# Kernel tuning notes

Measured on AMD Instinct MI355X. Metric: run time of the kernel, lower is better.

The kernel has to match this reference:

```python
import jax, jax.numpy as jnp
import numpy as np

B, S, D_IN, D_OUT = 4, 4096, 1024, 1024

def setup_inputs() -> dict:
    key = jax.random.key(0)
    kx, kq, kk, kv = jax.random.split(key, 4)
    # torch Linear weights are [out, in]; init scale ~ U(-1/sqrt(in), 1/sqrt(in))
    lim = 1.0 / np.sqrt(D_IN)
    x = jax.random.normal(kx, (B, S, D_IN), dtype=jnp.float32)
    W_query = jax.random.uniform(kq, (D_OUT, D_IN), dtype=jnp.float32, minval=-lim, maxval=lim)
    W_key = jax.random.uniform(kk, (D_OUT, D_IN), dtype=jnp.float32, minval=-lim, maxval=lim)
    W_value = jax.random.uniform(kv, (D_OUT, D_IN), dtype=jnp.float32, minval=-lim, maxval=lim)
    return {"x": x, "W_query": W_query, "W_key": W_key, "W_value": W_value}

def reference(x, W_query, W_key, W_value):
    # Linear: x @ W.T  (torch convention, weight shape [out, in])
    q = jnp.einsum('bsd,od->bso', x, W_query)
    k = jnp.einsum('bsd,od->bso', x, W_key)
    v = jnp.einsum('bsd,od->bso', x, W_value)
    scale = 1.0 / jnp.sqrt(jnp.asarray(k.shape[-1], dtype=x.dtype))
    scores = jnp.einsum('bqo,bko->bqk', q, k) * scale  # [B,S,S]
    weights = jax.nn.softmax(scores, axis=-1)
    return jnp.einsum('bqk,bko->bqo', weights, v)  # [B,S,D_OUT]
```

## Files before the change

### kernel.cpp

```cpp
#include <hip/hip_runtime.h>
#include <cstdint>
#include <cstddef>

typedef __attribute__((ext_vector_type(8))) short short8;
typedef __attribute__((ext_vector_type(4))) float f32x4;

__device__ __forceinline__ unsigned short f2bf(float x) {
  union { float f; unsigned u; } v; v.f = x;
  unsigned r = (v.u + 0x7FFFu + ((v.u >> 16) & 1u)) >> 16;
  return (unsigned short)r;
}

#define GLOAD16(g, l)                                                    \
  __builtin_amdgcn_global_load_lds(                                      \
      (const __attribute__((address_space(1))) unsigned int*)(g),        \
      (__attribute__((address_space(3))) unsigned int*)(l), 16, 0, 0)

#define DSR(dst, addrv, imm)                                             \
  asm volatile("ds_read_b128 %0, %1 offset:%c2"                          \
               : "=&v"(dst) : "v"(addrv), "i"(imm))

__global__ __launch_bounds__(256) void cvt_all(
    const float* __restrict__ x, unsigned short* __restrict__ xb,
    const float* __restrict__ wq, const float* __restrict__ wk,
    unsigned short* __restrict__ wqT, unsigned short* __restrict__ wkT,
    const float* __restrict__ wv, unsigned short* __restrict__ wvb) {
  __shared__ float tile[64][65];
  int b = blockIdx.x;
  int t = threadIdx.x;
  if (b < 8192) {
    long i = ((long)b * 256 + t) * 8;
    const float4* p = (const float4*)(x + i);
    float4 a = p[0], c = p[1];
    short8 r;
    r[0] = (short)f2bf(a.x); r[1] = (short)f2bf(a.y);
    r[2] = (short)f2bf(a.z); r[3] = (short)f2bf(a.w);
    r[4] = (short)f2bf(c.x); r[5] = (short)f2bf(c.y);
    r[6] = (short)f2bf(c.z); r[7] = (short)f2bf(c.w);
    *(short8*)(xb + i) = r;
  } else if (b < 8704) {
    int tb = b - 8192;
    const float* in = (tb & 256) ? wk : wq;
    unsigned short* out = (tb & 256) ? wkT : wqT;
    int tb2 = tb & 255;
    int O0 = (tb2 >> 4) * 64;
    int I0 = (tb2 & 15) * 64;
    int r0 = t >> 6, c = t & 63;
#pragma unroll
    for (int r = 0; r < 16; r++) {
      int row = r * 4 + r0;
      tile[row][c] = in[(size_t)(O0 + row) * 1024 + I0 + c];
    }
    __syncthreads();
#pragma unroll
    for (int r = 0; r < 16; r++) {
      int irow = r * 4 + r0;
      out[(size_t)(I0 + irow) * 1024 + O0 + c] = f2bf(tile[c][irow]);
    }
  } else {
    long i = ((long)(b - 8704) * 256 + t) * 8;
    const float4* p = (const float4*)(wv + i);
    float4 a = p[0], c = p[1];
    short8 r;
    r[0] = (short)f2bf(a.x); r[1] = (short)f2bf(a.y);
    r[2] = (short)f2bf(a.z); r[3] = (short)f2bf(a.w);
    r[4] = (short)f2bf(c.x); r[5] = (short)f2bf(c.y);
    r[6] = (short)f2bf(c.z); r[7] = (short)f2bf(c.w);
    *(short8*)(wvb + i) = r;
  }
}

__global__ __launch_bounds__(256) void reduce_rsum(
    const float* __restrict__ part, float* __restrict__ outr,
    size_t stride, int n) {
  int i = blockIdx.x * 256 + threadIdx.x;
  if (i >= n) return;
  float s = 0.f;
#pragma unroll
  for (int p = 0; p < 64; p++) s += part[(size_t)p * stride + i];
  outr[i] = 1.0f / s;
}

__global__ __launch_bounds__(256) void gemm128(
    const unsigned short* __restrict__ A, int lda,
    const unsigned short* __restrict__ B, int ldb,
    unsigned short* __restrict__ C, int ldc,
    int nbn, int K, float scale) {
  __shared__ unsigned short As[128 * 64];
  __shared__ unsigned short Bs[128 * 64];

  unsigned bid = blockIdx.x;
  unsigned cpx = gridDim.x >> 3;
  unsigned swz = (bid & 7u) * cpx + (bid >> 3);
  int bm = (int)(swz / (unsigned)nbn);
  int bn = (int)(swz % (unsigned)nbn);
  int m0 = bm * 128, n0 = bn * 128;

  int t = threadIdx.x;
  int lane = t & 63, wid = t >> 6;
  int wm = wid >> 1, wn = wid & 1;
  int l15 = lane & 15, l4 = lane >> 4;

  int srow = t >> 3;
  int g = (t & 7) ^ ((t >> 3) & 7);
  const unsigned short* pa = A + (size_t)(m0 + srow) * lda + g * 8;
  const unsigned short* pb = B + (size_t)(n0 + srow) * ldb + g * 8;

  f32x4 acc[4][4] = {};

  for (int k0 = 0; k0 < K; k0 += 64) {
    __syncthreads();
#pragma unroll
    for (int i = 0; i < 4; i++) {
      GLOAD16(pa + (size_t)(32 * i) * lda + k0,
              (char*)As + (size_t)(i * 256 + wid * 64) * 16);
      GLOAD16(pb + (size_t)(32 * i) * ldb + k0,
              (char*)Bs + (size_t)(i * 256 + wid * 64) * 16);
    }
    __syncthreads();
#pragma unroll
    for (int ks = 0; ks < 2; ks++) {
      short8 af[4], bfr[4];
#pragma unroll
      for (int mi = 0; mi < 4; mi++) {
        int r = wm * 64 + mi * 16 + l15;
        int c = ((ks << 2) | l4) ^ (r & 7);
        af[mi] = *(const short8*)((const char*)As + r * 128 + c * 16);
      }
#pragma unroll
      for (int ni = 0; ni < 4; ni++) {
        int r = wn * 64 + ni * 16 + l15;
        int c = ((ks << 2) | l4) ^ (r & 7);
        bfr[ni] = *(const short8*)((const char*)Bs + r * 128 + c * 16);
      }
#pragma unroll
      for (int mi = 0; mi < 4; mi++)
#pragma unroll
        for (int ni = 0; ni < 4; ni++)
          acc[mi][ni] = __builtin_amdgcn_mfma_f32_16x16x32_bf16(
              af[mi], bfr[ni], acc[mi][ni], 0, 0, 0);
    }
  }

#pragma unroll
  for (int mi = 0; mi < 4; mi++)
#pragma unroll
    for (int ni = 0; ni < 4; ni++)
#pragma unroll
      for (int j = 0; j < 4; j++) {
        int row = m0 + wm * 64 + mi * 16 + l4 * 4 + j;
        int col = n0 + wn * 64 + ni * 16 + l15;
        C[(size_t)row * ldc + col] = f2bf(acc[mi][ni][j] * scale);
      }
}

template <int MODE>
__device__ __forceinline__ void gemm_body(
    unsigned short (*As)[256 * 64], unsigned short (*Bs)[256 * 64],
    const unsigned short* __restrict__ A, int lda,
    const unsigned short* __restrict__ B, int ldb,
    void* __restrict__ Cb, int ldc,
    float* __restrict__ rs, size_t rsp,
    int nbn, int K, float scale, int stile) {
  unsigned bid = blockIdx.x;
  int bm, bn;
  if (stile) {
    unsigned xcd = bid & 7u, idx = bid >> 3;
    bm = (int)((xcd >> 1) * 4 + (idx & 3));
    bn = (int)((xcd & 1) * 8 + (idx >> 2));
  } else {
    unsigned cpx = gridDim.x >> 3;
    unsigned swz = (bid & 7u) * cpx + (bid >> 3);
    bm = (int)(swz / (unsigned)nbn);
    bn = (int)(swz % (unsigned)nbn);
  }
  int m0 = bm * 256, n0 = bn * 256;

  int t512 = threadIdx.x;
  int lane = t512 & 63, wid = t512 >> 6;
  int wm = wid >> 2, wn = wid & 3;
  int l15 = lane & 15, l4 = lane >> 4;

  int srow = t512 >> 3;
  int g = (t512 & 7) ^ ((t512 >> 3) & 7);
  const unsigned short* pa = A + (size_t)(m0 + srow) * lda + g * 8;
  const unsigned short* pb = B + (size_t)(n0 + srow) * ldb + g * 8;

  f32x4 acc[8][4] = {};

  const int NT = K >> 6;

#define STAGE(jj, buf)                                                    \
  do {                                                                    \
    int _k0 = (jj) << 6;                                                  \
    _Pragma("unroll") for (int i = 0; i < 4; i++)                         \
        GLOAD16(pa + (size_t)(i * 64) * lda + _k0,                        \
                (char*)As[buf] + i * 8192 + t512 * 16);                   \
    _Pragma("unroll") for (int i = 0; i < 4; i++)                         \
        GLOAD16(pb + (size_t)(i * 64) * ldb + _k0,                        \
                (char*)Bs[buf] + i * 8192 + t512 * 16);                   \
  } while (0)

  unsigned c0 = ((unsigned)l4) ^ (unsigned)(l15 & 7);
  unsigned c1 = (4u | (unsigned)l4) ^ (unsigned)(l15 & 7);
  unsigned rowA = (unsigned)(wm * 128 + l15) * 128u;
  unsigned rowB = (unsigned)(wn * 64 + l15) * 128u;

  STAGE(0, 0);

  for (int j = 0; j < NT; ++j) {
    int cur = j & 1;
    __builtin_amdgcn_sched_barrier(0);
    __builtin_amdgcn_s_barrier();
    if (j + 1 < NT) {
      STAGE(j + 1, cur ^ 1);
      asm volatile("s_waitcnt vmcnt(8)" ::: "memory");
    } else {
      asm volatile("s_waitcnt vmcnt(0)" ::: "memory");
    }
    __builtin_amdgcn_s_barrier();

    unsigned baseA = (unsigned)(uintptr_t)(
        (__attribute__((address_space(3))) char*)(&As[cur][0]));
    unsigned baseB = (unsigned)(uintptr_t)(
        (__attribute__((address_space(3))) char*)(&Bs[cur][0]));
    unsigned aA0 = baseA + rowA + c0 * 16, aA1 = baseA + rowA + c1 * 16;
    unsigned aB0 = baseB + rowB + c0 * 16, aB1 = baseB + rowB + c1 * 16;

    short8 afq[2][2][2];
    short8 bfv[4][2];

    DSR(afq[0][0][0], aA0, 0);
    DSR(afq[0][0][1], aA1, 0);
    DSR(afq[0][1][0], aA0, 2048);
    DSR(afq[0][1][1], aA1, 2048);
#pragma unroll
    for (int ni = 0; ni < 4; ni++) {
      DSR(bfv[ni][0], aB0, ni * 2048);
      DSR(bfv[ni][1], aB1, ni * 2048);
    }

#pragma unroll
    for (int p = 0; p < 4; ++p) {
      if (p < 3) {
        const int mi0 = (p + 1) * 2;
        DSR(afq[(p + 1) & 1][0][0], aA0, mi0 * 2048);
        DSR(afq[(p + 1) & 1][0][1], aA1, mi0 * 2048);
        DSR(afq[(p + 1) & 1][1][0], aA0, (mi0 + 1) * 2048);
        DSR(afq[(p + 1) & 1][1][1], aA1, (mi0 + 1) * 2048);
        asm volatile("s_waitcnt lgkmcnt(4)" ::: "memory");
      } else {
        asm volatile("s_waitcnt lgkmcnt(0)" ::: "memory");
      }
      __builtin_amdgcn_sched_barrier(0);
      __builtin_amdgcn_s_setprio(1);
#pragma unroll
      for (int ks = 0; ks < 2; ks++)
#pragma unroll
        for (int m2 = 0; m2 < 2; m2++) {
          int mi = p * 2 + m2;
#pragma unroll
          for (int ni = 0; ni < 4; ni++)
            acc[mi][ni] = __builtin_amdgcn_mfma_f32_16x16x32_bf16(
                afq[p & 1][m2][ks], bfv[ni][ks], acc[mi][ni], 0, 0, 0);
        }
      __builtin_amdgcn_s_setprio(0);
      __builtin_amdgcn_sched_barrier(0);
    }
  }
#undef STAGE

  if constexpr (MODE == 2) {
    float sums[8][4];
#pragma unroll
    for (int mi = 0; mi < 8; mi++)
#pragma unroll
      for (int jj = 0; jj < 4; jj++) sums[mi][jj] = 0.f;
#pragma unroll
    for (int mi = 0; mi < 8; mi++)
#pragma unroll
      for (int ni = 0; ni < 4; ni++)
#pragma unroll
        for (int jj = 0; jj < 4; jj++) {
          int row = m0 + wm * 128 + mi * 16 + l4 * 4 + jj;
          int col = n0 + wn * 64 + ni * 16 + l15;
          float e = __expf(acc[mi][ni][jj] * scale);
          sums[mi][jj] += e;
          ((unsigned short*)Cb)[(size_t)row * ldc + col] = f2bf(e);
        }
    size_t pslot = (size_t)(bn * 4 + wn) * rsp;
#pragma unroll
    for (int mi = 0; mi < 8; mi++)
#pragma unroll
      for (int jj = 0; jj < 4; jj++) {
        float s = sums[mi][jj];
        s += __shfl_xor(s, 1);
        s += __shfl_xor(s, 2);
        s += __shfl_xor(s, 4);
        s += __shfl_xor(s, 8);
        if (l15 == 0) {
          int row = m0 + wm * 128 + mi * 16 + l4 * 4 + jj;
          rs[pslot + row] = s;
        }
      }
  } else {
#pragma unroll
    for (int mi = 0; mi < 8; mi++) {
      float inv[4];
      if constexpr (MODE == 3) {
#pragma unroll
        for (int jj = 0; jj < 4; jj++) {
          int row = m0 + wm * 128 + mi * 16 + l4 * 4 + jj;
          inv[jj] = rs[row];
        }
      }
#pragma unroll
      for (int ni = 0; ni < 4; ni++)
#pragma unroll
        for (int jj = 0; jj < 4; jj++) {
          int row = m0 + wm * 128 + mi * 16 + l4 * 4 + jj;
          int col = n0 + wn * 64 + ni * 16 + l15;
          float val = acc[mi][ni][jj];
          if constexpr (MODE == 1)
            ((unsigned short*)Cb)[(size_t)row * ldc + col] = f2bf(val * scale);
          else
            ((float*)Cb)[(size_t)row * ldc + col] = val * inv[jj];
        }
    }
  }
}

template <int MODE, int STILE>
__global__ __launch_bounds__(512, 2) void gemm_bt256(
    const unsigned short* __restrict__ A, int lda, size_t asb,
    const unsigned short* __restrict__ B, int ldb, size_t bsb,
    void* __restrict__ C, int ldc, size_t csb,
    float* __restrict__ rs, int rss, size_t rsp,
    int nbn, int K, float scale) {
  __shared__ unsigned short As[2][256 * 64];
  __shared__ unsigned short Bs[2][256 * 64];
  gemm_body<MODE>(As, Bs,
                  A + (size_t)blockIdx.y * asb, lda,
                  B + (size_t)blockIdx.y * bsb, ldb,
                  (char*)C + (size_t)blockIdx.y * csb * (MODE == 3 ? 4 : 2),
                  ldc, rs + (size_t)blockIdx.y * rss, rsp, nbn, K, scale,
                  STILE);
}

__global__ __launch_bounds__(512, 2) void gemm_dual(
    const unsigned short* __restrict__ A0, int lda0,
    const unsigned short* __restrict__ B0, int ldb0,
    void* __restrict__ C0, int ldc0, int nbn0,
    const unsigned short* __restrict__ A1, int lda1,
    const unsigned short* __restrict__ B1, int ldb1,
    void* __restrict__ C1, int ldc1, int nbn1, int K) {
  __shared__ unsigned short As[2][256 * 64];
  __shared__ unsigned short Bs[2][256 * 64];
  if (blockIdx.y == 0)
    gemm_body<1>(As, Bs, A0, lda0, B0, ldb0, C0, ldc0, nullptr, 0, nbn0, K,
                 1.0f, 0);
  else
    gemm_body<1>(As, Bs, A1, lda1, B1, ldb1, C1, ldc1, nullptr, 0, nbn1, K,
                 1.0f, 0);
}

extern "C" void kernel_launch(void* const* d_in, const int* in_sizes, int n_in,
                              void* d_out, int out_size, void* d_ws, size_t ws_size,
                              hipStream_t stream) {
  (void)in_sizes; (void)n_in; (void)out_size;
  const float* x  = (const float*)d_in[0];
  const float* Wq = (const float*)d_in[1];
  const float* Wk = (const float*)d_in[2];
  const float* Wv = (const float*)d_in[3];
  float* out = (float*)d_out;

  const int Bn = 4, S = 4096, D = 1024;
  const size_t MS = (size_t)Bn * S;
  const float scale = 0.03125f;

  char* ws = (char*)d_ws;
  unsigned short* xb  = (unsigned short*)ws; ws += MS * D * 2;
  unsigned short* xMb = (unsigned short*)ws; ws += MS * D * 2;
  unsigned short* VTb = (unsigned short*)ws; ws += MS * D * 2;
  unsigned short* Sreg = (unsigned short*)ws;
  const size_t s4_bytes = (size_t)Bn * S * S * 2;
  const size_t s1_bytes = (size_t)S * S * 2;
  size_t head = (size_t)(ws - (char*)d_ws);
  bool batched = ws_size >= head + s4_bytes + 16u * 1024 * 1024;
  ws += batched ? s4_bytes : s1_bytes;
  unsigned short* wqT = (unsigned short*)ws; ws += (size_t)D * D * 2;
  unsigned short* wkT = (unsigned short*)ws; ws += (size_t)D * D * 2;
  unsigned short* MTb = (unsigned short*)ws; ws += (size_t)D * D * 2;
  unsigned short* wvb = (unsigned short*)ws; ws += (size_t)D * D * 2;
  float* rpart = (float*)ws; ws += 64 * MS * sizeof(float);
  float* rinv  = (float*)ws;

  cvt_all<<<9216, 256, 0, stream>>>(x, xb, Wq, Wk, wqT, wkT, Wv, wvb);

  gemm128<<<64, 256, 0, stream>>>(wkT, D, wqT, D, MTb, D, 8, D, 1.0f);

  gemm_dual<<<dim3(256, 2), 512, 0, stream>>>(
      wvb, D, xb, D, VTb, (int)MS, 64,
      xb, D, MTb, D, xMb, D, 4, D);

  if (batched) {
    gemm_bt256<2, 1><<<dim3(256, Bn), 512, 0, stream>>>(
        xMb, D, (size_t)S * D,
        xb, D, (size_t)S * D,
        Sreg, S, (size_t)S * S, rpart, S, MS, 16, D, scale);
    reduce_rsum<<<(int)(MS / 256), 256, 0, stream>>>(rpart, rinv, MS, (int)MS);
    gemm_bt256<3, 0><<<dim3(64, Bn), 512, 0, stream>>>(
        Sreg, S, (size_t)S * S,
        VTb, (int)MS, (size_t)S,
        out, D, (size_t)S * D, rinv, S, 0, 4, S, 1.0f);
  } else {
    for (int b = 0; b < Bn; b++) {
      gemm_bt256<2, 1><<<dim3(256, 1), 512, 0, stream>>>(
          xMb + (size_t)b * S * D, D, 0,
          xb + (size_t)b * S * D, D, 0,
          Sreg, S, 0, rpart + (size_t)b * S, 0, MS, 16, D, scale);
      reduce_rsum<<<S / 256, 256, 0, stream>>>(
          rpart + (size_t)b * S, rinv + (size_t)b * S, MS, S);
      gemm_bt256<3, 0><<<dim3(64, 1), 512, 0, stream>>>(
          Sreg, S, 0, VTb + (size_t)b * S, (int)MS, 0,
          out + (size_t)b * S * D, D, 0, rinv + (size_t)b * S, 0, 0,
          4, S, 1.0f);
    }
  }
}
```

Baseline: 398.3 us.

## Split-K the weight-product GEMM into eight partial blocks plus reduction

The 1024x1024 Wk^T·Wq product previously ran as a single 64-block GEMM that underfilled the GPU. It now splits K into eight 128-wide chunks across a second grid dimension, writes fp32 partials into the score scratch region, and sums them in a separate reduction kernel that converts to bf16. This raises parallelism at the cost of an extra launch and 32 MB of partial-sum traffic. The result also moves from a single fp32 accumulation to an fp32 sum of partials.

```diff
diff --git a/kernel.cpp b/kernel.cpp
--- a/kernel.cpp
+++ b/kernel.cpp
@@ -3,6 +3,7 @@
 #include <cstddef>
 
 typedef __attribute__((ext_vector_type(8))) short short8;
+typedef __attribute__((ext_vector_type(4))) short short4v;
 typedef __attribute__((ext_vector_type(4))) float f32x4;
 
 __device__ __forceinline__ unsigned short f2bf(float x) {
@@ -81,20 +82,21 @@
   outr[i] = 1.0f / s;
 }
 
-__global__ __launch_bounds__(256) void gemm128(
-    const unsigned short* __restrict__ A, int lda,
-    const unsigned short* __restrict__ B, int ldb,
-    unsigned short* __restrict__ C, int ldc,
-    int nbn, int K, float scale) {
+__global__ __launch_bounds__(256) void mt_part(
+    const unsigned short* __restrict__ A,
+    const unsigned short* __restrict__ B,
+    float* __restrict__ P) {
   __shared__ unsigned short As[128 * 64];
   __shared__ unsigned short Bs[128 * 64];
+  const int lda = 1024, ldb = 1024;
 
   unsigned bid = blockIdx.x;
   unsigned cpx = gridDim.x >> 3;
   unsigned swz = (bid & 7u) * cpx + (bid >> 3);
-  int bm = (int)(swz / (unsigned)nbn);
-  int bn = (int)(swz % (unsigned)nbn);
+  int bm = (int)(swz >> 3);
+  int bn = (int)(swz & 7u);
   int m0 = bm * 128, n0 = bn * 128;
+  int kbase = (int)blockIdx.y << 7;
 
   int t = threadIdx.x;
   int lane = t & 63, wid = t >> 6;
@@ -103,12 +105,12 @@
 
   int srow = t >> 3;
   int g = (t & 7) ^ ((t >> 3) & 7);
-  const unsigned short* pa = A + (size_t)(m0 + srow) * lda + g * 8;
-  const unsigned short* pb = B + (size_t)(n0 + srow) * ldb + g * 8;
+  const unsigned short* pa = A + (size_t)(m0 + srow) * lda + g * 8 + kbase;
+  const unsigned short* pb = B + (size_t)(n0 + srow) * ldb + g * 8 + kbase;
 
   f32x4 acc[4][4] = {};
 
-  for (int k0 = 0; k0 < K; k0 += 64) {
+  for (int k0 = 0; k0 < 128; k0 += 64) {
     __syncthreads();
 #pragma unroll
     for (int i = 0; i < 4; i++) {
@@ -142,6 +144,7 @@
     }
   }
 
+  float* out = P + (size_t)blockIdx.y * 1048576;
 #pragma unroll
   for (int mi = 0; mi < 4; mi++)
 #pragma unroll
@@ -150,8 +153,23 @@
       for (int j = 0; j < 4; j++) {
         int row = m0 + wm * 64 + mi * 16 + l4 * 4 + j;
         int col = n0 + wn * 64 + ni * 16 + l15;
-        C[(size_t)row * ldc + col] = f2bf(acc[mi][ni][j] * scale);
-      }
+        out[(size_t)row * 1024 + col] = acc[mi][ni][j];
+      }
+}
+
+__global__ __launch_bounds__(256) void mt_reduce(
+    const float* __restrict__ P, unsigned short* __restrict__ M) {
+  size_t i = ((size_t)blockIdx.x * 256 + threadIdx.x) * 4;
+  float4 s = *(const float4*)(P + i);
+#pragma unroll
+  for (int c = 1; c < 8; c++) {
+    float4 v = *(const float4*)(P + (size_t)c * 1048576 + i);
+    s.x += v.x; s.y += v.y; s.z += v.z; s.w += v.w;
+  }
+  short4v r;
+  r[0] = (short)f2bf(s.x); r[1] = (short)f2bf(s.y);
+  r[2] = (short)f2bf(s.z); r[3] = (short)f2bf(s.w);
+  *(short4v*)(M + i) = r;
 }
 
 template <int MODE>
@@ -394,10 +412,12 @@
   unsigned short* wvb = (unsigned short*)ws; ws += (size_t)D * D * 2;
   float* rpart = (float*)ws; ws += 64 * MS * sizeof(float);
   float* rinv  = (float*)ws;
+  float* mtp = (float*)Sreg;
 
   cvt_all<<<9216, 256, 0, stream>>>(x, xb, Wq, Wk, wqT, wkT, Wv, wvb);
 
-  gemm128<<<64, 256, 0, stream>>>(wkT, D, wqT, D, MTb, D, 8, D, 1.0f);
+  mt_part<<<dim3(64, 8), 256, 0, stream>>>(wkT, wqT, mtp);
+  mt_reduce<<<1024, 256, 0, stream>>>(mtp, MTb);
 
   gemm_dual<<<dim3(256, 2), 512, 0, stream>>>(
       wvb, D, xb, D, VTb, (int)MS, 64,
```

New measurement: 396.0 us. About the same (-0.6%).
